# Kernel tuning notes

Measured on AMD Instinct MI355X. Metric: run time of the kernel, lower is better.

## Reference

```python
import jax, jax.numpy as jnp
import numpy as np

# Model / shape constants (match init_kwargs and input_specs)
E, H, N, B = 1024, 16, 4096, 4
D = E // H               # head_dim = 64
W_SZ, EXT, C_SZ = 128, 128, 128   # window, ext window, rf chunk
NEG = -1e9


def _linear(x, w, b):
    # torch nn.Linear convention: w is (out, in)
    return x @ w.T + b


def _layernorm(x, g, b, eps=1e-5):
    m = jnp.mean(x, -1, keepdims=True)
    v = jnp.mean((x - m) ** 2, -1, keepdims=True)
    return (x - m) * jax.lax.rsqrt(v + eps) * g + b


def _ext_windows(x, w, ext):
    # x: (b,h,n,d) -> (b,h,g,ext+w,d); window g covers keys [g*w-ext, g*w+w)
    # (front-padded with zeros, same as causal_window_1d_partition + as_strided)
    g = x.shape[2] // w
    xp = jnp.pad(x, ((0, 0), (0, 0), (ext, 0), (0, 0)))
    idx = jnp.arange(g)[:, None] * w + jnp.arange(ext + w)[None, :]
    return xp[:, :, idx]


def setup_inputs() -> dict:
    key = jax.random.key(0)
    ks = jax.random.split(key, 20)
    p = lambda i, shape: jax.random.normal(ks[i], shape, jnp.float32) * 0.02
    return {
        'query': jax.random.normal(ks[0], (N, B, E), jnp.float32),
        'Wq': p(1, (E, E)), 'bq': jnp.zeros((E,), jnp.float32),
        'Wk': p(2, (E, E)), 'bk': jnp.zeros((E,), jnp.float32),
        'Wv': p(3, (E, E)), 'bv': jnp.zeros((E,), jnp.float32),
        'Wo': p(4, (E, E)), 'bo': jnp.zeros((E,), jnp.float32),
        'mu_q_w': p(5, (D, D)), 'mu_q_b': jnp.zeros((D,), jnp.float32),
        'mu_q_g': jnp.ones((D,), jnp.float32), 'mu_q_be': jnp.zeros((D,), jnp.float32),
        'mu_k_w': p(6, (D, D)), 'mu_k_b': jnp.zeros((D,), jnp.float32),
        'mu_k_g': jnp.ones((D,), jnp.float32), 'mu_k_be': jnp.zeros((D,), jnp.float32),
    }


def reference(query, Wq, bq, Wk, bk, Wv, bv, Wo, bo,
              mu_q_w, mu_q_b, mu_q_g, mu_q_be,
              mu_k_w, mu_k_b, mu_k_g, mu_k_be):
    n, b, e = query.shape
    h, d = H, D
    scaling = d ** -0.5

    q = _linear(query, Wq, bq)
    k = _linear(query, Wk, bk)
    v = _linear(query, Wv, bv)
    to_bhnd = lambda t: jnp.transpose(t.reshape(n, b, h, d), (1, 2, 0, 3))
    q, k, v = to_bhnd(q), to_bhnd(k), to_bhnd(v)
    q = q * scaling

    # ---------------- local causal windowed attention scores ----------------
    g = n // W_SZ
    w_q = q.reshape(b, h, g, W_SZ, d)
    w_k = _ext_windows(k, W_SZ, EXT)   # (b,h,g,EXT+W,d)
    w_v = _ext_windows(v, W_SZ, EXT)
    local_dots = jnp.einsum('bhgid,bhgjd->bhgij', w_q, w_k)
    i = jnp.arange(W_SZ)[:, None]
    j = jnp.arange(EXT + W_SZ)[None, :]
    causal_ok = j <= i + EXT                      # key pos <= query pos
    gi = jnp.arange(g)[:, None, None]
    valid = j[None] >= (EXT - gi * W_SZ)          # mask zero-padded front keys
    local_mask = causal_ok[None] & valid          # (g, W, EXT+W)
    local_dots = jnp.where(local_mask[None, None], local_dots, NEG)

    # ------------- random-feature (EVA) chunk-level global branch -------------
    nc = n // C_SZ
    rf_q = q.reshape(b, h, nc, C_SZ, d)
    rf_k = k.reshape(b, h, nc, C_SZ, d)
    rf_v = v.reshape(b, h, nc, C_SZ, d)
    rf_q_bar = _layernorm(_linear(rf_q.mean(-2), mu_q_w, mu_q_b), mu_q_g, mu_q_be)
    rf_k_bar = _layernorm(_linear(rf_k.mean(-2), mu_k_w, mu_k_b), mu_k_g, mu_k_be)
    mu = rf_q_bar + rf_k_bar   # eval mode: weights = mu (no Gaussian noise)

    # prm_projection(rf_k, mu) with normalize=False, then softmax within chunk
    norm = scaling * jnp.sum(rf_k ** 2, -1) / 2.0            # (b,h,nc,p)
    log_proj_k = jnp.einsum('bhcd,bhcpd->bhcp', mu, rf_k) * scaling - norm
    beta = jax.nn.softmax(log_proj_k, -1)
    rfa_chunk = jnp.einsum('bhcp,bhcpd->bhcd', beta, rf_v)   # SNIS chunk values

    rfa_dots = jnp.einsum('bhgid,bhcd->bhgic', w_q, rf_k_bar)
    # chunk c visible to window g iff the whole chunk precedes the window
    chunk_vis = (jnp.arange(nc)[None, :] + 1) * C_SZ <= jnp.arange(g)[:, None] * W_SZ
    rfa_dots = jnp.where(chunk_vis[None, None, :, None, :], rfa_dots, NEG)

    # joint softmax over [local keys | global chunk pseudo-keys]
    attn = jax.nn.softmax(jnp.concatenate([local_dots, rfa_dots], -1), -1)
    la, ga = attn[..., : EXT + W_SZ], attn[..., EXT + W_SZ:]
    out = jnp.einsum('bhgij,bhgjd->bhgid', la, w_v) \
        + jnp.einsum('bhgic,bhcd->bhgid', ga, rfa_chunk)

    out = out.reshape(b, h, n, d)
    out = jnp.transpose(out, (2, 0, 1, 3)).reshape(n, b, e)
    return _linear(out, Wo, bo)
```

## Files before the change

### kernel.cpp

```cpp
#include <hip/hip_runtime.h>
#include <hip/hip_bf16.h>

typedef __hip_bfloat16 bf16;
typedef __attribute__((ext_vector_type(8))) short bf16x8;
typedef __attribute__((ext_vector_type(4))) float f32x4;

#define E_DIM 1024
#define H_DIM 16
#define N_DIM 4096
#define B_DIM 4
#define D_DIM 64
#define G_WIN 32
#define NC 32
#define M_ROWS 16384

#define AS1 __attribute__((address_space(1)))
#define AS3 __attribute__((address_space(3)))

__global__ __launch_bounds__(256) void cvt_f32_bf16(
    const float* __restrict__ in, bf16* __restrict__ out)
{
    int i = (blockIdx.x * 256 + threadIdx.x) * 8;
    float4 f0 = *(const float4*)(in + i);
    float4 f1 = *(const float4*)(in + i + 4);
    union { bf16 t[8]; uint4 u; } pk;
    pk.t[0] = (bf16)f0.x; pk.t[1] = (bf16)f0.y; pk.t[2] = (bf16)f0.z; pk.t[3] = (bf16)f0.w;
    pk.t[4] = (bf16)f1.x; pk.t[5] = (bf16)f1.y; pk.t[6] = (bf16)f1.z; pk.t[7] = (bf16)f1.w;
    *(uint4*)(out + i) = pk.u;
}

template<int MODE, bool WB16>
__global__ __launch_bounds__(256) void gemm_mfma(
    const bf16* __restrict__ A, const void* __restrict__ Wp,
    const float* __restrict__ bias, float scale,
    bf16* __restrict__ out_bf, float* __restrict__ out_f,
    bf16* __restrict__ out_k, bf16* __restrict__ out_v)
{
    __shared__ bf16 As[128 * 32];
    __shared__ bf16 Bs[128 * 32];
    int tid  = threadIdx.x;
    int lane = tid & 63;
    int wv   = tid >> 6;
    int wm   = (wv >> 1) * 64;
    int wn   = (wv & 1) * 64;
    int quad = lane >> 4;
    int l16  = lane & 15;

    int chunk  = blockIdx.x & 7;
    int lc     = blockIdx.x >> 3;
    int colt   = lc >> 4;
    int rowsub = lc & 15;
    int col0 = colt * 128;
    int row0 = (chunk * 16 + rowsub) * 128;

    f32x4 acc[4][4] = {};

    for (int k0 = 0; k0 < E_DIM; k0 += 32) {
#pragma unroll
        for (int i = 0; i < 2; i++) {
            int idx = tid + i * 256;
            int r = idx >> 2, c = idx & 3;
            const bf16* g = A + (size_t)(row0 + r) * E_DIM + k0 + c * 8;
            __builtin_amdgcn_global_load_lds(
                (const AS1 void*)g, (AS3 void*)(As + idx * 8), 16, 0, 0);
        }
        if constexpr (WB16) {
            const bf16* Wb = (const bf16*)Wp;
#pragma unroll
            for (int i = 0; i < 2; i++) {
                int idx = tid + i * 256;
                int e = idx >> 2, c = idx & 3;
                const bf16* g = Wb + (size_t)(col0 + e) * E_DIM + k0 + c * 8;
                __builtin_amdgcn_global_load_lds(
                    (const AS1 void*)g, (AS3 void*)(Bs + idx * 8), 16, 0, 0);
            }
        } else {
            const float* Wf = (const float*)Wp;
#pragma unroll
            for (int i = 0; i < 2; i++) {
                int idx = tid + i * 256;
                int e = idx >> 2, c = idx & 3;
                const float* wr = Wf + (size_t)(col0 + e) * E_DIM + k0 + c * 8;
                float4 f0 = *(const float4*)wr;
                float4 f1 = *(const float4*)(wr + 4);
                union { bf16 t[8]; uint4 u; } pk;
                pk.t[0] = (bf16)f0.x; pk.t[1] = (bf16)f0.y;
                pk.t[2] = (bf16)f0.z; pk.t[3] = (bf16)f0.w;
                pk.t[4] = (bf16)f1.x; pk.t[5] = (bf16)f1.y;
                pk.t[6] = (bf16)f1.z; pk.t[7] = (bf16)f1.w;
                *(uint4*)(Bs + idx * 8) = pk.u;
            }
        }
        __syncthreads();

        bf16x8 af[4], bfr[4];
#pragma unroll
        for (int t = 0; t < 4; t++) {
            af[t]  = *(const bf16x8*)(As + (wm + t * 16 + l16) * 32 + quad * 8);
            bfr[t] = *(const bf16x8*)(Bs + (wn + t * 16 + l16) * 32 + quad * 8);
        }
#pragma unroll
        for (int mt = 0; mt < 4; mt++)
#pragma unroll
            for (int nt = 0; nt < 4; nt++)
                acc[mt][nt] = __builtin_amdgcn_mfma_f32_16x16x32_bf16(
                    af[mt], bfr[nt], acc[mt][nt], 0, 0, 0);
        __syncthreads();
    }

    bf16* dst = out_bf;
    float scl = scale;
    if (MODE == 2) {
        int sel = col0 >> 10;
        dst = (sel == 0) ? out_bf : ((sel == 1) ? out_k : out_v);
        scl = (sel == 0) ? scale : 1.0f;
    }

#pragma unroll
    for (int mt = 0; mt < 4; mt++)
#pragma unroll
        for (int nt = 0; nt < 4; nt++)
#pragma unroll
            for (int rg = 0; rg < 4; rg++) {
                int m = row0 + wm + mt * 16 + quad * 4 + rg;
                int e = col0 + wn + nt * 16 + l16;
                float val = acc[mt][nt][rg];
                if (MODE == 1) {
                    out_f[(size_t)m * E_DIM + e] = val + bias[e];
                } else {
                    float v2 = (val + bias[e]) * scl;
                    int el = e & 1023;
                    int n = m >> 2, bb = m & 3;
                    int h = el >> 6, d = el & 63;
                    dst[((((size_t)bb * H_DIM + h) * N_DIM + n) * D_DIM) + d] = (bf16)v2;
                }
            }
}

__global__ __launch_bounds__(128) void chunk_stats(
    const bf16* __restrict__ q_s, const bf16* __restrict__ kbuf, const bf16* __restrict__ vbuf,
    const float* __restrict__ mqw, const float* __restrict__ mqb,
    const float* __restrict__ mqg, const float* __restrict__ mqbe,
    const float* __restrict__ mkw, const float* __restrict__ mkb,
    const float* __restrict__ mkg, const float* __restrict__ mkbe,
    float* __restrict__ rf_k_bar, float* __restrict__ rfa_chunk)
{
    int bid = blockIdx.x;
    int c = bid % NC;
    int bh = bid / NC;
    int tid = threadIdx.x;
    int lane = tid & 63;
    int wid = tid >> 6;

    __shared__ float qm[64], km[64], mu_s[64], sc[128];
    __shared__ float parts[4];

    size_t base = ((size_t)bh * N_DIM + c * 128) * D_DIM;

    if (tid < 64) {
        float s = 0.f;
        for (int p = 0; p < 128; p++) s += (float)q_s[base + p * 64 + tid];
        qm[tid] = s * (1.0f / 128.0f);
    } else {
        int d = tid - 64;
        float s = 0.f;
        for (int p = 0; p < 128; p++) s += (float)kbuf[base + p * 64 + d];
        km[d] = s * (1.0f / 128.0f);
    }
    __syncthreads();

    {
        float t;
        if (wid == 0) {
            t = mqb[lane];
            for (int d2 = 0; d2 < 64; d2++) t += qm[d2] * mqw[lane * 64 + d2];
        } else {
            t = mkb[lane];
            for (int d2 = 0; d2 < 64; d2++) t += km[d2] * mkw[lane * 64 + d2];
        }
        float s = t;
        s += __shfl_xor(s, 1);  s += __shfl_xor(s, 2);  s += __shfl_xor(s, 4);
        s += __shfl_xor(s, 8);  s += __shfl_xor(s, 16); s += __shfl_xor(s, 32);
        float mean = s * (1.0f / 64.0f);
        float x = t - mean;
        float v2 = x * x;
        v2 += __shfl_xor(v2, 1);  v2 += __shfl_xor(v2, 2);  v2 += __shfl_xor(v2, 4);
        v2 += __shfl_xor(v2, 8);  v2 += __shfl_xor(v2, 16); v2 += __shfl_xor(v2, 32);
        float rstd = rsqrtf(v2 * (1.0f / 64.0f) + 1e-5f);
        if (wid == 0) {
            qm[lane] = x * rstd * mqg[lane] + mqbe[lane];
        } else {
            float kn = x * rstd * mkg[lane] + mkbe[lane];
            km[lane] = kn;
            rf_k_bar[(size_t)bh * NC * 64 + c * 64 + lane] = kn;
        }
    }
    __syncthreads();
    if (tid < 64) mu_s[tid] = qm[tid] + km[tid];
    __syncthreads();

    float scv;
    {
        float dot = 0.f, ss = 0.f;
        const bf16* kr = kbuf + base + tid * 64;
        for (int d = 0; d < 64; d++) {
            float kv = (float)kr[d];
            dot += mu_s[d] * kv;
            ss += kv * kv;
        }
        scv = dot * 0.125f - 0.0625f * ss;
    }
    {
        float mv = scv;
        mv = fmaxf(mv, __shfl_xor(mv, 1));  mv = fmaxf(mv, __shfl_xor(mv, 2));
        mv = fmaxf(mv, __shfl_xor(mv, 4));  mv = fmaxf(mv, __shfl_xor(mv, 8));
        mv = fmaxf(mv, __shfl_xor(mv, 16)); mv = fmaxf(mv, __shfl_xor(mv, 32));
        if (lane == 0) parts[wid] = mv;
        __syncthreads();
        float mall = fmaxf(parts[0], parts[1]);
        float e = expf(scv - mall);
        float sv = e;
        sv += __shfl_xor(sv, 1);  sv += __shfl_xor(sv, 2);  sv += __shfl_xor(sv, 4);
        sv += __shfl_xor(sv, 8);  sv += __shfl_xor(sv, 16); sv += __shfl_xor(sv, 32);
        if (lane == 0) parts[2 + wid] = sv;
        __syncthreads();
        float inv = 1.0f / (parts[2] + parts[3]);
        sc[tid] = e * inv;
    }
    __syncthreads();

    if (tid < 64) {
        float acc = 0.f;
        for (int p = 0; p < 128; p++) acc += sc[p] * (float)vbuf[base + p * 64 + tid];
        rfa_chunk[(size_t)bh * NC * 64 + c * 64 + tid] = acc;
    }
}

__global__ __launch_bounds__(512, 4) void attn_kernel(
    const bf16* __restrict__ qin, const bf16* __restrict__ kbuf, const bf16* __restrict__ vbuf,
    const float* __restrict__ rf_k_bar, const float* __restrict__ rfa_chunk,
    bf16* __restrict__ aout)
{
    int bid = blockIdx.x;
    int g = bid & (G_WIN - 1);
    int bh = bid / G_WIN;
    int b = bh >> 4, h = bh & 15;
    int tid = threadIdx.x;
    int lane = tid & 63;
    int wv = tid >> 6;
    int q4 = lane >> 4;
    int l16 = lane & 15;

    __shared__ __align__(16) short Ks[288 * 72];
    __shared__ __align__(16) short Vt[64 * 296];

    size_t kvbase = (size_t)bh * N_DIM * D_DIM;
    int k0g = g * 128 - 128;

#pragma unroll
    for (int i = 0; i < 4; i++) {
        int ci = tid + i * 512;
        int key = ci >> 3, chc = ci & 7;
        int kidx = k0g + key; if (kidx < 0) kidx = 0;
        bf16x8 v = *(const bf16x8*)(kbuf + kvbase + (size_t)kidx * 64 + chc * 8);
        *(bf16x8*)(Ks + key * 72 + chc * 8) = v;
    }
    if (tid < 256) {
        int c = tid >> 3, chc = tid & 7;
        const float* src = rf_k_bar + (size_t)bh * NC * 64 + c * 64 + chc * 8;
        float4 f0 = *(const float4*)src;
        float4 f1 = *(const float4*)(src + 4);
        union { bf16 t[8]; bf16x8 v; } pk;
        pk.t[0] = (bf16)f0.x; pk.t[1] = (bf16)f0.y;
        pk.t[2] = (bf16)f0.z; pk.t[3] = (bf16)f0.w;
        pk.t[4] = (bf16)f1.x; pk.t[5] = (bf16)f1.y;
        pk.t[6] = (bf16)f1.z; pk.t[7] = (bf16)f1.w;
        *(bf16x8*)(Ks + (256 + c) * 72 + chc * 8) = pk.v;
    }
#pragma unroll
    for (int i = 0; i < 4; i++) {
        int ci = tid + i * 512;
        int key = ci & 255, dc = ci >> 8;
        int kidx = k0g + key; if (kidx < 0) kidx = 0;
        union { bf16x8 v; short s[8]; } u;
        u.v = *(const bf16x8*)(vbuf + kvbase + (size_t)kidx * 64 + dc * 8);
        int colp = (key & ~31) | (((key >> 2) & 3) << 3)
                 | (((key >> 4) & 1) << 2) | (key & 3);
#pragma unroll
        for (int jj = 0; jj < 8; jj++)
            Vt[(dc * 8 + jj) * 296 + colp] = u.s[jj];
    }
    if (tid < 256) {
        int d = tid >> 2, cg = tid & 3;
        const float* rc = rfa_chunk + (size_t)bh * NC * 64;
#pragma unroll
        for (int jj = 0; jj < 8; jj++) {
            int c = cg * 8 + jj;
            int p = (((c >> 2) & 3) << 3) | (((c >> 4) & 1) << 2) | (c & 3);
            union { bf16 bv; short s; } cv;
            cv.bv = (bf16)rc[(size_t)c * 64 + d];
            Vt[d * 296 + 256 + p] = cv.s;
        }
    }

    bf16x8 bq0, bq1;
    {
        const bf16* qrow = qin + kvbase + (size_t)(g * 128 + wv * 16 + l16) * 64 + q4 * 8;
        bq0 = *(const bf16x8*)qrow;
        bq1 = *(const bf16x8*)(qrow + 32);
    }

    __syncthreads();

    f32x4 acc[18] = {};
    __builtin_amdgcn_s_setprio(1);
#pragma unroll
    for (int ct = 0; ct < 18; ct++) {
        bool live = (ct < 16) ? (ct <= wv + 8 && !(g == 0 && ct < 8))
                              : ((ct == 16) ? (g > 0) : (g > 16));
        if (!live) continue;
        int r = ct * 16 + l16;
        bf16x8 ak0 = *(const bf16x8*)(Ks + r * 72 + q4 * 8);
        bf16x8 ak1 = *(const bf16x8*)(Ks + r * 72 + 32 + q4 * 8);
        acc[ct] = __builtin_amdgcn_mfma_f32_16x16x32_bf16(ak0, bq0, acc[ct], 0, 0, 0);
        acc[ct] = __builtin_amdgcn_mfma_f32_16x16x32_bf16(ak1, bq1, acc[ct], 0, 0, 0);
    }
    __builtin_amdgcn_s_setprio(0);

    int qi = wv * 16 + l16;
    float m = -1e30f;
#pragma unroll
    for (int ct = 0; ct < 18; ct++) {
        bool live = (ct < 16) ? (ct <= wv + 8 && !(g == 0 && ct < 8))
                              : ((ct == 16) ? (g > 0) : (g > 16));
        if (!live) continue;
        int jbase = ct * 16 + q4 * 4;
#pragma unroll
        for (int rg = 0; rg < 4; rg++) {
            int j = jbase + rg;
            bool ok = (j < 256) ? (k0g + j >= 0 && j <= qi + 128) : ((j - 256) < g);
            float s = ok ? acc[ct][rg] : -1e9f;
            acc[ct][rg] = s;
            m = fmaxf(m, s);
        }
    }
    m = fmaxf(m, __shfl_xor(m, 16));
    m = fmaxf(m, __shfl_xor(m, 32));

    float sum = 0.f;
#pragma unroll
    for (int ct = 0; ct < 18; ct++) {
        bool live = (ct < 16) ? (ct <= wv + 8 && !(g == 0 && ct < 8))
                              : ((ct == 16) ? (g > 0) : (g > 16));
        if (!live) continue;
#pragma unroll
        for (int rg = 0; rg < 4; rg++) {
            float p = __expf(acc[ct][rg] - m);
            acc[ct][rg] = p;
            sum += p;
        }
    }
    sum += __shfl_xor(sum, 16);
    sum += __shfl_xor(sum, 32);
    float rinv = 1.0f / sum;

    f32x4 accO[4] = {};
    __builtin_amdgcn_s_setprio(1);
#pragma unroll
    for (int cc = 0; cc < 9; cc++) {
        bool live = (cc < 8) ? (2 * cc <= wv + 8 && !(g == 0 && cc < 4)) : (g > 0);
        if (!live) continue;
        union { bf16 t[8]; bf16x8 v; } pb;
#pragma unroll
        for (int e = 0; e < 4; e++) {
            pb.t[e]     = (bf16)acc[2 * cc][e];
            pb.t[4 + e] = (bf16)acc[2 * cc + 1][e];
        }
#pragma unroll
        for (int dt = 0; dt < 4; dt++) {
            bf16x8 av = *(const bf16x8*)(Vt + (dt * 16 + l16) * 296 + (cc * 4 + q4) * 8);
            accO[dt] = __builtin_amdgcn_mfma_f32_16x16x32_bf16(av, pb.v, accO[dt], 0, 0, 0);
        }
    }
    __builtin_amdgcn_s_setprio(0);

    int nn = g * 128 + wv * 16 + l16;
    size_t obase = ((size_t)nn * B_DIM + b) * E_DIM + h * 64;
#pragma unroll
    for (int dt = 0; dt < 4; dt++) {
        union { bf16 t[4]; uint2 u; } o;
#pragma unroll
        for (int rg = 0; rg < 4; rg++) o.t[rg] = (bf16)(accO[dt][rg] * rinv);
        *(uint2*)(aout + obase + dt * 16 + q4 * 4) = o.u;
    }
}

extern "C" void kernel_launch(void* const* d_in, const int* in_sizes, int n_in,
                              void* d_out, int out_size, void* d_ws, size_t ws_size,
                              hipStream_t stream) {
    const float* query = (const float*)d_in[0];
    const float* Wq   = (const float*)d_in[1];
    const float* bq   = (const float*)d_in[2];
    const float* Wk   = (const float*)d_in[3];
    const float* bk   = (const float*)d_in[4];
    const float* Wv   = (const float*)d_in[5];
    const float* bv   = (const float*)d_in[6];
    const float* Wo   = (const float*)d_in[7];
    const float* bo   = (const float*)d_in[8];
    const float* mqw  = (const float*)d_in[9];
    const float* mqb  = (const float*)d_in[10];
    const float* mqg  = (const float*)d_in[11];
    const float* mqbe = (const float*)d_in[12];
    const float* mkw  = (const float*)d_in[13];
    const float* mkb  = (const float*)d_in[14];
    const float* mkg  = (const float*)d_in[15];
    const float* mkbe = (const float*)d_in[16];

    const size_t SZ = (size_t)B_DIM * H_DIM * N_DIM * D_DIM;
    const size_t STATS = (size_t)B_DIM * H_DIM * NC * D_DIM;

    bf16* kb = (bf16*)d_ws;
    bf16* vb = kb + SZ;
    float* rf_k_bar  = (float*)(vb + SZ);
    float* rfa_chunk = rf_k_bar + STATS;

    size_t base_bytes = 2 * SZ * sizeof(bf16) + 2 * STATS * sizeof(float);
    size_t wmat = (size_t)E_DIM * E_DIM;
    size_t wb16_bytes = base_bytes + 4 * wmat * sizeof(bf16) + 3072 * sizeof(float);
    bool wb16   = ws_size >= wb16_bytes;
    bool big_ws = ws_size >= wb16_bytes + SZ * sizeof(bf16);
    bf16* wq_b = (bf16*)((char*)d_ws + base_bytes);
    bf16* wk_b = wq_b + wmat;
    bf16* wv_b = wk_b + wmat;
    bf16* wo_b = wv_b + wmat;
    float* biasQKV = (float*)(wo_b + wmat);
    bf16* att_ws = (bf16*)(biasQKV + 3072);

    float* outf = (float*)d_out;
    bf16* qb  = (bf16*)d_out;
    bf16* qbf = qb + SZ;

    dim3 gblk(256);
    int ggrd1 = (E_DIM / 128) * (M_ROWS / 128);
    int ggrd3 = 3 * ggrd1;

    cvt_f32_bf16<<<(M_ROWS * E_DIM) / (256 * 8), 256, 0, stream>>>(query, qbf);
    if (wb16) {
        int wblk = (int)(wmat / (256 * 8));
        cvt_f32_bf16<<<wblk, 256, 0, stream>>>(Wq, wq_b);
        cvt_f32_bf16<<<wblk, 256, 0, stream>>>(Wk, wk_b);
        cvt_f32_bf16<<<wblk, 256, 0, stream>>>(Wv, wv_b);
        cvt_f32_bf16<<<wblk, 256, 0, stream>>>(Wo, wo_b);
        (void)hipMemcpyAsync(biasQKV,        bq, 1024 * sizeof(float), hipMemcpyDeviceToDevice, stream);
        (void)hipMemcpyAsync(biasQKV + 1024, bk, 1024 * sizeof(float), hipMemcpyDeviceToDevice, stream);
        (void)hipMemcpyAsync(biasQKV + 2048, bv, 1024 * sizeof(float), hipMemcpyDeviceToDevice, stream);
    }

    if (wb16) {
        gemm_mfma<2, true><<<ggrd3, gblk, 0, stream>>>(
            qbf, wq_b, biasQKV, 0.125f, qb, nullptr, kb, vb);
    } else {
        gemm_mfma<0, false><<<ggrd1, gblk, 0, stream>>>(qbf, Wq, bq, 0.125f, qb, nullptr, nullptr, nullptr);
        gemm_mfma<0, false><<<ggrd1, gblk, 0, stream>>>(qbf, Wk, bk, 1.0f, kb, nullptr, nullptr, nullptr);
        gemm_mfma<0, false><<<ggrd1, gblk, 0, stream>>>(qbf, Wv, bv, 1.0f, vb, nullptr, nullptr, nullptr);
    }

    chunk_stats<<<B_DIM * H_DIM * NC, 128, 0, stream>>>(
        qb, kb, vb, mqw, mqb, mqg, mqbe, mkw, mkb, mkg, mkbe, rf_k_bar, rfa_chunk);

    bf16* attn_dst = big_ws ? att_ws : qbf;
    attn_kernel<<<B_DIM * H_DIM * G_WIN, 512, 0, stream>>>(
        qb, kb, vb, rf_k_bar, rfa_chunk, attn_dst);

    const bf16* gemm_in;
    if (big_ws) {
        gemm_in = att_ws;
    } else {
        (void)hipMemcpyAsync(kb, qbf, SZ * sizeof(bf16), hipMemcpyDeviceToDevice, stream);
        gemm_in = kb;
    }

    if (wb16) {
        gemm_mfma<1, true><<<ggrd1, gblk, 0, stream>>>(gemm_in, wo_b, bo, 1.0f, nullptr, outf, nullptr, nullptr);
    } else {
        gemm_mfma<1, false><<<ggrd1, gblk, 0, stream>>>(gemm_in, Wo, bo, 1.0f, nullptr, outf, nullptr, nullptr);
    }
}
```

Measured before the change: 403.0 us.

## Double GEMM K-tile with XOR-swizzled LDS and fuse conversion launches

The bf16 MFMA GEMM now stages a 64-wide K tile per iteration instead of 32, halving the number of barrier pairs, and XOR-swizzles the 16-byte column slots in LDS to avoid bank conflicts on fragment reads. Separately, the query, four weight conversions and three bias copies are merged into a single launch to cut launch and memcpy overhead. LDS use per block doubles, which may reduce occupancy.

```diff
diff --git a/kernel.cpp b/kernel.cpp
--- a/kernel.cpp
+++ b/kernel.cpp
@@ -17,16 +17,44 @@
 #define AS1 __attribute__((address_space(1)))
 #define AS3 __attribute__((address_space(3)))
 
-__global__ __launch_bounds__(256) void cvt_f32_bf16(
-    const float* __restrict__ in, bf16* __restrict__ out)
-{
-    int i = (blockIdx.x * 256 + threadIdx.x) * 8;
+__device__ __forceinline__ void cvt8(const float* __restrict__ in,
+                                     bf16* __restrict__ out, int blk) {
+    int i = (blk * 256 + (int)threadIdx.x) * 8;
     float4 f0 = *(const float4*)(in + i);
     float4 f1 = *(const float4*)(in + i + 4);
     union { bf16 t[8]; uint4 u; } pk;
     pk.t[0] = (bf16)f0.x; pk.t[1] = (bf16)f0.y; pk.t[2] = (bf16)f0.z; pk.t[3] = (bf16)f0.w;
     pk.t[4] = (bf16)f1.x; pk.t[5] = (bf16)f1.y; pk.t[6] = (bf16)f1.z; pk.t[7] = (bf16)f1.w;
     *(uint4*)(out + i) = pk.u;
+}
+
+__global__ __launch_bounds__(256) void cvt_f32_bf16(
+    const float* __restrict__ in, bf16* __restrict__ out)
+{
+    cvt8(in, out, blockIdx.x);
+}
+
+__global__ __launch_bounds__(256) void cvt_all(
+    const float* __restrict__ q, bf16* __restrict__ qo,
+    const float* __restrict__ w0, const float* __restrict__ w1,
+    const float* __restrict__ w2, const float* __restrict__ w3,
+    bf16* __restrict__ o0, bf16* __restrict__ o1,
+    bf16* __restrict__ o2, bf16* __restrict__ o3,
+    const float* __restrict__ bq, const float* __restrict__ bk,
+    const float* __restrict__ bv, float* __restrict__ biasQKV)
+{
+    int bid = blockIdx.x;
+    if (bid < 8192) {
+        cvt8(q, qo, bid);
+    } else if (bid < 10240) {
+        int wi = (bid - 8192) >> 9, off = (bid - 8192) & 511;
+        const float* src = (wi == 0) ? w0 : (wi == 1) ? w1 : (wi == 2) ? w2 : w3;
+        bf16* dst = (wi == 0) ? o0 : (wi == 1) ? o1 : (wi == 2) ? o2 : o3;
+        cvt8(src, dst, off);
+    } else {
+        for (int i = threadIdx.x; i < 3072; i += 256)
+            biasQKV[i] = (i < 1024) ? bq[i] : (i < 2048) ? bk[i - 1024] : bv[i - 2048];
+    }
 }
 
 template<int MODE, bool WB16>
@@ -36,8 +64,8 @@
     bf16* __restrict__ out_bf, float* __restrict__ out_f,
     bf16* __restrict__ out_k, bf16* __restrict__ out_v)
 {
-    __shared__ bf16 As[128 * 32];
-    __shared__ bf16 Bs[128 * 32];
+    __shared__ bf16 As[128 * 64];
+    __shared__ bf16 Bs[128 * 64];
     int tid  = threadIdx.x;
     int lane = tid & 63;
     int wv   = tid >> 6;
@@ -45,6 +73,7 @@
     int wn   = (wv & 1) * 64;
     int quad = lane >> 4;
     int l16  = lane & 15;
+    int x7   = l16 & 7;
 
     int chunk  = blockIdx.x & 7;
     int lc     = blockIdx.x >> 3;
@@ -55,32 +84,32 @@
 
     f32x4 acc[4][4] = {};
 
-    for (int k0 = 0; k0 < E_DIM; k0 += 32) {
-#pragma unroll
-        for (int i = 0; i < 2; i++) {
+    for (int k0 = 0; k0 < E_DIM; k0 += 64) {
+#pragma unroll
+        for (int i = 0; i < 4; i++) {
             int idx = tid + i * 256;
-            int r = idx >> 2, c = idx & 3;
-            const bf16* g = A + (size_t)(row0 + r) * E_DIM + k0 + c * 8;
+            int r = idx >> 3, s = idx & 7;
+            const bf16* g = A + (size_t)(row0 + r) * E_DIM + k0 + ((s ^ (r & 7)) * 8);
             __builtin_amdgcn_global_load_lds(
                 (const AS1 void*)g, (AS3 void*)(As + idx * 8), 16, 0, 0);
         }
         if constexpr (WB16) {
             const bf16* Wb = (const bf16*)Wp;
 #pragma unroll
-            for (int i = 0; i < 2; i++) {
+            for (int i = 0; i < 4; i++) {
                 int idx = tid + i * 256;
-                int e = idx >> 2, c = idx & 3;
-                const bf16* g = Wb + (size_t)(col0 + e) * E_DIM + k0 + c * 8;
+                int r = idx >> 3, s = idx & 7;
+                const bf16* g = Wb + (size_t)(col0 + r) * E_DIM + k0 + ((s ^ (r & 7)) * 8);
                 __builtin_amdgcn_global_load_lds(
                     (const AS1 void*)g, (AS3 void*)(Bs + idx * 8), 16, 0, 0);
             }
         } else {
             const float* Wf = (const float*)Wp;
 #pragma unroll
-            for (int i = 0; i < 2; i++) {
+            for (int i = 0; i < 4; i++) {
                 int idx = tid + i * 256;
-                int e = idx >> 2, c = idx & 3;
-                const float* wr = Wf + (size_t)(col0 + e) * E_DIM + k0 + c * 8;
+                int r = idx >> 3, s = idx & 7;
+                const float* wr = Wf + (size_t)(col0 + r) * E_DIM + k0 + ((s ^ (r & 7)) * 8);
                 float4 f0 = *(const float4*)wr;
                 float4 f1 = *(const float4*)(wr + 4);
                 union { bf16 t[8]; uint4 u; } pk;
@@ -93,18 +122,22 @@
         }
         __syncthreads();
 
-        bf16x8 af[4], bfr[4];
-#pragma unroll
-        for (int t = 0; t < 4; t++) {
-            af[t]  = *(const bf16x8*)(As + (wm + t * 16 + l16) * 32 + quad * 8);
-            bfr[t] = *(const bf16x8*)(Bs + (wn + t * 16 + l16) * 32 + quad * 8);
-        }
-#pragma unroll
-        for (int mt = 0; mt < 4; mt++)
-#pragma unroll
-            for (int nt = 0; nt < 4; nt++)
-                acc[mt][nt] = __builtin_amdgcn_mfma_f32_16x16x32_bf16(
-                    af[mt], bfr[nt], acc[mt][nt], 0, 0, 0);
+#pragma unroll
+        for (int kc = 0; kc < 2; kc++) {
+            int cs = kc * 4 + quad;
+            bf16x8 af[4], bfr[4];
+#pragma unroll
+            for (int t = 0; t < 4; t++) {
+                af[t]  = *(const bf16x8*)(As + (wm + t * 16 + l16) * 64 + ((cs ^ x7) * 8));
+                bfr[t] = *(const bf16x8*)(Bs + (wn + t * 16 + l16) * 64 + ((cs ^ x7) * 8));
+            }
+#pragma unroll
+            for (int mt = 0; mt < 4; mt++)
+#pragma unroll
+                for (int nt = 0; nt < 4; nt++)
+                    acc[mt][nt] = __builtin_amdgcn_mfma_f32_16x16x32_bf16(
+                        af[mt], bfr[nt], acc[mt][nt], 0, 0, 0);
+        }
         __syncthreads();
     }
 
@@ -444,16 +477,12 @@
     int ggrd1 = (E_DIM / 128) * (M_ROWS / 128);
     int ggrd3 = 3 * ggrd1;
 
-    cvt_f32_bf16<<<(M_ROWS * E_DIM) / (256 * 8), 256, 0, stream>>>(query, qbf);
     if (wb16) {
-        int wblk = (int)(wmat / (256 * 8));
-        cvt_f32_bf16<<<wblk, 256, 0, stream>>>(Wq, wq_b);
-        cvt_f32_bf16<<<wblk, 256, 0, stream>>>(Wk, wk_b);
-        cvt_f32_bf16<<<wblk, 256, 0, stream>>>(Wv, wv_b);
-        cvt_f32_bf16<<<wblk, 256, 0, stream>>>(Wo, wo_b);
-        (void)hipMemcpyAsync(biasQKV,        bq, 1024 * sizeof(float), hipMemcpyDeviceToDevice, stream);
-        (void)hipMemcpyAsync(biasQKV + 1024, bk, 1024 * sizeof(float), hipMemcpyDeviceToDevice, stream);
-        (void)hipMemcpyAsync(biasQKV + 2048, bv, 1024 * sizeof(float), hipMemcpyDeviceToDevice, stream);
+        cvt_all<<<10241, 256, 0, stream>>>(
+            query, qbf, Wq, Wk, Wv, Wo, wq_b, wk_b, wv_b, wo_b,
+            bq, bk, bv, biasQKV);
+    } else {
+        cvt_f32_bf16<<<(M_ROWS * E_DIM) / (256 * 8), 256, 0, stream>>>(query, qbf);
     }
 
     if (wb16) {
```

New measurement: 400.7 us. No clear change (-0.6%).
